# Kernel optimization log

Hardware: AMD Instinct MI355X
Metric: run time of the kernel (lower is better)

## Reference

```python
import jax, jax.numpy as jnp
import numpy as np

D_MODEL = 1024
N_HEADS = 16
D_K = D_MODEL // N_HEADS
THETA = 10000.0
BATCH, SEQ = 4, 2048


def apply_rope(x, pos, theta=THETA):
    # x: [B, H, S, d_k]; pos: [S] int. Rotate interleaved pairs (x_{2i}, x_{2i+1}).
    half = x.shape[-1] // 2
    inv_freq = theta ** (-jnp.arange(half, dtype=x.dtype) * 2.0 / x.shape[-1])  # [half]
    ang = pos.astype(x.dtype)[:, None] * inv_freq[None, :]                      # [S, half]
    cos, sin = jnp.cos(ang), jnp.sin(ang)
    x1, x2 = x[..., 0::2], x[..., 1::2]
    r1 = x1 * cos - x2 * sin
    r2 = x1 * sin + x2 * cos
    return jnp.stack([r1, r2], axis=-1).reshape(x.shape)


def setup_inputs() -> dict:
    key = jax.random.key(0)
    k1, k2, k3 = jax.random.split(key, 3)
    x = jax.random.normal(k1, (BATCH, SEQ, D_MODEL), dtype=jnp.float32)
    W_qkv = jax.random.normal(k2, (3 * D_MODEL, D_MODEL), dtype=jnp.float32) * (D_MODEL ** -0.5)
    b_qkv = jnp.zeros((3 * D_MODEL,), dtype=jnp.float32)
    W_o = jax.random.normal(k3, (D_MODEL, D_MODEL), dtype=jnp.float32) * (D_MODEL ** -0.5)
    b_o = jnp.zeros((D_MODEL,), dtype=jnp.float32)
    token_positions = jnp.arange(SEQ, dtype=jnp.int64 if jax.config.jax_enable_x64 else jnp.int32)
    return {"x": x, "token_positions": token_positions, "W_qkv": W_qkv,
            "b_qkv": b_qkv, "W_o": W_o, "b_o": b_o}


def reference(x, token_positions, W_qkv, b_qkv, W_o, b_o):
    B, S, _ = x.shape
    qkv = x @ W_qkv.T + b_qkv                                   # [B, S, 3*d_model]
    qkv = qkv.reshape(B, S, 3, N_HEADS, D_K)
    qkv = jnp.transpose(qkv, (2, 0, 3, 1, 4))                   # [3, B, H, S, d_k]
    q, k, v = qkv[0], qkv[1], qkv[2]
    q = apply_rope(q, token_positions)
    k = apply_rope(k, token_positions)
    scores = jnp.einsum('bhqd,bhkd->bhqk', q / jnp.sqrt(jnp.asarray(D_K, x.dtype)), k)
    causal = jnp.tril(jnp.ones((S, S), dtype=bool))             # True where attended
    scores = jnp.where(causal, scores, jnp.asarray(-jnp.inf, scores.dtype))
    attn = jax.nn.softmax(scores, axis=-1)
    out = jnp.einsum('bhqk,bhkd->bhqd', attn, v)                # [B, H, S, d_k]
    out = jnp.transpose(out, (0, 2, 1, 3)).reshape(B, S, D_MODEL)
    return out @ W_o.T + b_o
```

## Files before the change

kernel.cpp:

```cpp
#include <hip/hip_runtime.h>
#include <hip/hip_bf16.h>
#include <cstdint>

#define S_LEN 2048
#define NHEAD 16
#define DMODEL 1024

using short8 = __attribute__((ext_vector_type(8))) short;
using f32x4  = __attribute__((ext_vector_type(4))) float;

__device__ __forceinline__ float bf2f(ushort u) {
    return __uint_as_float(((uint32_t)u) << 16);
}
__device__ __forceinline__ ushort f2bf(float f) {
    uint32_t u = __float_as_uint(f);
    u += 0x7FFF + ((u >> 16) & 1);
    return (ushort)(u >> 16);
}
__device__ __forceinline__ uint32_t cvt_pk_bf16(float lo, float hi) {
    uint32_t r;
    asm("v_cvt_pk_bf16_f32 %0, %1, %2" : "=v"(r) : "v"(lo), "v"(hi));
    return r;
}
__device__ __forceinline__ float exp2_(float x) {
    float r; asm("v_exp_f32 %0, %1" : "=v"(r) : "v"(x)); return r;
}
template<int N> __device__ __forceinline__ void vwait() {
    asm volatile("s_waitcnt vmcnt(%0)" :: "n"(N) : "memory");
}

__global__ void k_cast(const float* __restrict__ in, ushort* __restrict__ out, int n4) {
    int i = blockIdx.x * blockDim.x + threadIdx.x;
    if (i < n4) {
        const float4 v = reinterpret_cast<const float4*>(in)[i];
        ushort4 o;
        o.x = f2bf(v.x); o.y = f2bf(v.y); o.z = f2bf(v.z); o.w = f2bf(v.w);
        reinterpret_cast<ushort4*>(out)[i] = o;
    }
}

__device__ __forceinline__ void gl16(const ushort* g, ushort* l) {
    __builtin_amdgcn_global_load_lds(
        (const __attribute__((address_space(1))) void*)g,
        (__attribute__((address_space(3))) void*)l, 16, 0, 0);
}

__global__ __launch_bounds__(512, 2)
void k_gemm256(const ushort* __restrict__ A, const ushort* __restrict__ Bm,
               const float* __restrict__ bias, ushort* __restrict__ C,
               int M, int N, int K, int nbn)
{
    __shared__ ushort As[2][16384];
    __shared__ ushort Bs[2][16384];

    const int bid = blockIdx.x;
    const int cpx = gridDim.x >> 3;
    const int wg = (bid & 7) * cpx + (bid >> 3);
    const int bn = (wg % nbn) * 256, bm = (wg / nbn) * 256;
    const int t = threadIdx.x, w = t >> 6, l = t & 63;
    const int wr = w >> 2, wc = w & 3;
    const int lr = l & 15, lg = l >> 4;

    f32x4 acc[8][4] = {};

    auto stage_pair = [&](int kt, int b, int u0) {
        #pragma unroll
        for (int uu = 0; uu < 2; ++uu) {
            const int u = u0 + uu;
            const int e = (u & 3) * 4096 + t * 8;
            const int r = e >> 6;
            const int c = (e & 63) ^ ((r & 7) << 3);
            if (u < 4) gl16(Bm + (size_t)(bn + r) * K + kt * 64 + c, &Bs[b][e]);
            else       gl16(A  + (size_t)(bm + r) * K + kt * 64 + c, &As[b][e]);
        }
    };

    const int NT = K >> 6;

    stage_pair(0, 0, 0); stage_pair(0, 0, 2);
    stage_pair(0, 0, 4); stage_pair(0, 0, 6);
    if (NT > 1) {
        stage_pair(1, 1, 0); stage_pair(1, 1, 2);
        vwait<4>();
    } else {
        vwait<0>();
    }
    __builtin_amdgcn_s_barrier();

    short8 bfr[4][2];

    for (int tt = 0; tt < NT; ++tt) {
        const int b = tt & 1;
        const ushort* Al = As[b];
        const ushort* Bl = Bs[b];

        #pragma unroll
        for (int p = 0; p < 4; ++p) {
            if (p == 0) {
                #pragma unroll
                for (int n = 0; n < 4; ++n) {
                    const int rB = wc * 64 + n * 16 + lr;
                    #pragma unroll
                    for (int kk = 0; kk < 2; ++kk)
                        bfr[n][kk] = *(const short8*)&Bl[rB * 64 + ((kk * 32 + lg * 8) ^ ((rB & 7) << 3))];
                }
            }
            short8 afr[2][2];
            #pragma unroll
            for (int jj = 0; jj < 2; ++jj) {
                const int rA = wr * 16 + 32 * (2 * p + jj) + lr;
                #pragma unroll
                for (int kk = 0; kk < 2; ++kk)
                    afr[jj][kk] = *(const short8*)&Al[rA * 64 + ((kk * 32 + lg * 8) ^ ((rA & 7) << 3))];
            }
            if      (p == 0) { if (tt + 1 < NT) stage_pair(tt + 1, b ^ 1, 4); }
            else if (p == 1) { if (tt + 1 < NT) stage_pair(tt + 1, b ^ 1, 6); }
            else if (p == 2) { if (tt + 2 < NT) stage_pair(tt + 2, b, 0); }
            else             { if (tt + 2 < NT) stage_pair(tt + 2, b, 2); }

            __builtin_amdgcn_s_barrier();
            __builtin_amdgcn_s_setprio(1);
            #pragma unroll
            for (int jj = 0; jj < 2; ++jj)
                #pragma unroll
                for (int n = 0; n < 4; ++n)
                    #pragma unroll
                    for (int kk = 0; kk < 2; ++kk)
                        acc[2 * p + jj][n] = __builtin_amdgcn_mfma_f32_16x16x32_bf16(
                            afr[jj][kk], bfr[n][kk], acc[2 * p + jj][n], 0, 0, 0);
            __builtin_amdgcn_s_setprio(0);
            if (p == 3) {
                if      (tt + 2 < NT) vwait<4>();
                else if (tt + 1 < NT) vwait<0>();
            }
            __builtin_amdgcn_s_barrier();
        }
    }

    const int col0 = bn + wc * 64 + lr;
    float bv[4];
    #pragma unroll
    for (int n = 0; n < 4; ++n) bv[n] = bias[col0 + n * 16];
    #pragma unroll
    for (int j = 0; j < 8; ++j) {
        const int row0 = bm + wr * 16 + 32 * j + lg * 4;
        #pragma unroll
        for (int r = 0; r < 4; ++r) {
            const size_t ro = (size_t)(row0 + r) * N;
            #pragma unroll
            for (int n = 0; n < 4; ++n)
                C[ro + col0 + n * 16] = f2bf(acc[j][n][r] + bv[n]);
        }
    }
}

__global__ __launch_bounds__(256, 2)
void k_gemm_bt(const ushort* __restrict__ A, const ushort* __restrict__ Bm,
               const float* __restrict__ bias, float* __restrict__ Cout,
               int M, int N, int K)
{
    __shared__ ushort As[128 * 32];
    __shared__ ushort Bs[128 * 32];
    const int t = threadIdx.x;
    const int w = t >> 6, l = t & 63;
    const int lr = l & 15, lg = l >> 4;
    const int bm = blockIdx.y * 128, bn = blockIdx.x * 128;
    const int wr = (w >> 1) * 64, wc = (w & 1) * 64;

    f32x4 acc[4][4] = {};

    const ushort* ag = A + (size_t)(bm + (t >> 2)) * K + (t & 3) * 8;
    const ushort* bg = Bm + (size_t)(bn + (t >> 2)) * K + (t & 3) * 8;
    ushort* asd = &As[t * 8];
    ushort* bsd = &Bs[t * 8];
    const size_t rowskip = (size_t)64 * K;

    for (int k0 = 0; k0 < K; k0 += 32) {
        gl16(ag + k0, asd);
        gl16(ag + rowskip + k0, asd + 2048);
        gl16(bg + k0, bsd);
        gl16(bg + rowskip + k0, bsd + 2048);
        __syncthreads();
        short8 af[4], bf[4];
        #pragma unroll
        for (int m = 0; m < 4; ++m)
            af[m] = *reinterpret_cast<const short8*>(&As[(wr + m * 16 + lr) * 32 + lg * 8]);
        #pragma unroll
        for (int n = 0; n < 4; ++n)
            bf[n] = *reinterpret_cast<const short8*>(&Bs[(wc + n * 16 + lr) * 32 + lg * 8]);
        #pragma unroll
        for (int m = 0; m < 4; ++m)
            #pragma unroll
            for (int n = 0; n < 4; ++n)
                acc[m][n] = __builtin_amdgcn_mfma_f32_16x16x32_bf16(af[m], bf[n], acc[m][n], 0, 0, 0);
        __syncthreads();
    }

    const int col0 = bn + wc + lr;
    float bv[4];
    #pragma unroll
    for (int n = 0; n < 4; ++n) bv[n] = bias[col0 + n * 16];
    #pragma unroll
    for (int m = 0; m < 4; ++m) {
        const int row0 = bm + wr + m * 16 + lg * 4;
        #pragma unroll
        for (int r = 0; r < 4; ++r) {
            const size_t ro = (size_t)(row0 + r) * N;
            #pragma unroll
            for (int n = 0; n < 4; ++n)
                Cout[ro + col0 + n * 16] = acc[m][n][r] + bv[n];
        }
    }
}

__global__ __launch_bounds__(256)
void k_rope_scatter(const ushort* __restrict__ qkv, const int* __restrict__ pos,
                    ushort* __restrict__ Qo, ushort* __restrict__ Ko, ushort* __restrict__ Vt)
{
    __shared__ ushort vlds[64][72];
    const int blk = blockIdx.x;
    const int st = blk & 31, bh = blk >> 5;
    const int b = bh >> 4, h = bh & 15;
    const int t = threadIdx.x;
    const int sl = t >> 2, dc = (t & 3) << 4;
    const int s = st * 64 + sl;
    const size_t base = (size_t)(b * S_LEN + s) * 3072 + h * 64 + dc;
    const float p = (float)pos[s];

    float cs[8], sn[8];
    #pragma unroll
    for (int j = 0; j < 8; ++j) {
        const int fi = (dc >> 1) + j;
        const float invf = __expf(-(float)fi * 0.28782313662425572f);
        __sincosf(p * invf, &sn[j], &cs[j]);
    }

    #pragma unroll
    for (int type = 0; type < 2; ++type) {
        union { uint4 u[2]; ushort us[16]; } in_, out_;
        in_.u[0] = *(const uint4*)(qkv + base + type * 1024);
        in_.u[1] = *(const uint4*)(qkv + base + type * 1024 + 8);
        const float scale = (type == 0) ? 0.125f * 1.44269504088896f : 1.0f;
        #pragma unroll
        for (int j = 0; j < 8; ++j) {
            float x1 = bf2f(in_.us[2 * j]), x2 = bf2f(in_.us[2 * j + 1]);
            out_.us[2 * j]     = f2bf((x1 * cs[j] - x2 * sn[j]) * scale);
            out_.us[2 * j + 1] = f2bf((x1 * sn[j] + x2 * cs[j]) * scale);
        }
        ushort* dst = (type == 0 ? Qo : Ko) + ((size_t)(bh * S_LEN + s)) * 64 + dc;
        *(uint4*)dst = out_.u[0];
        *(uint4*)(dst + 8) = out_.u[1];
    }

    {
        uint4 v0 = *(const uint4*)(qkv + base + 2048);
        uint4 v1 = *(const uint4*)(qkv + base + 2048 + 8);
        *(uint4*)&vlds[sl][dc] = v0;
        *(uint4*)&vlds[sl][dc + 8] = v1;
    }
    __syncthreads();
    {
        const int d = t >> 2, sc0 = (t & 3) << 4;
        union { uint4 u[2]; ushort us[16]; } o;
        #pragma unroll
        for (int j = 0; j < 16; ++j) o.us[j] = vlds[sc0 + j][d];
        ushort* dst = Vt + ((size_t)bh * 64 + d) * S_LEN + st * 64 + sc0;
        *(uint4*)dst = o.u[0];
        *(uint4*)(dst + 8) = o.u[1];
    }
}

__global__ __launch_bounds__(256, 3)
void k_attn(const ushort* __restrict__ Q, const ushort* __restrict__ Kk,
            const ushort* __restrict__ Vt, ushort* __restrict__ O)
{
    __shared__ ushort Ks[2][4096];
    __shared__ ushort Vs[2][4096];
    __shared__ ushort P[4][32][72];

    const int blk = blockIdx.x;
    const int qb = 15 - (blk >> 6);
    const int bh = blk & 63;
    const int b = bh >> 4, h = bh & 15;
    const int t = threadIdx.x, w = t >> 6, l = t & 63;
    const int lr = l & 15, lg = l >> 4;

    const ushort* Kb = Kk + (size_t)bh * S_LEN * 64;
    const ushort* Vb = Vt + (size_t)bh * 64 * S_LEN;
    const ushort* Qb = Q + (size_t)bh * S_LEN * 64;

    const int qbase0 = qb * 128 + w * 16;
    const int qbase1 = qbase0 + 64;

    short8 qf[2][2];
    #pragma unroll
    for (int qg = 0; qg < 2; ++qg)
        #pragma unroll
        for (int dh = 0; dh < 2; ++dh)
            qf[qg][dh] = *(const short8*)(Qb + (size_t)(qbase0 + qg * 64 + lr) * 64 + dh * 32 + lg * 8);

    f32x4 acc[2][4] = {};
    float mx[2] = {-INFINITY, -INFINITY}, ls[2] = {0.f, 0.f};

    const int nt = 2 * qb + 2;

    auto stage = [&](int kb2, int buf) {
        ushort* Kd = Ks[buf]; ushort* Vd = Vs[buf];
        #pragma unroll
        for (int j = 0; j < 2; ++j) {
            const int e = (j * 256 + t) * 8;
            const int row = e >> 6;
            const int col = (e & 63) ^ ((row & 7) << 3);
            gl16(Kb + (size_t)(kb2 + row) * 64 + col, Kd + e);
            gl16(Vb + (size_t)row * S_LEN + kb2 + col, Vd + e);
        }
    };

    stage(0, 0);
    __syncthreads();

    for (int kt = 0; kt < nt; ++kt) {
        const int cur = kt & 1;
        const int kb = kt * 64;
        if (kt + 1 < nt) stage(kb + 64, cur ^ 1);

        const ushort* Kl = Ks[cur];
        short8 kf[4][2];
        #pragma unroll
        for (int i = 0; i < 4; ++i) {
            const int krow = i * 16 + lr, sw = (krow & 7) << 3;
            kf[i][0] = *(const short8*)&Kl[krow * 64 + ((lg * 8) ^ sw)];
            kf[i][1] = *(const short8*)&Kl[krow * 64 + ((32 + lg * 8) ^ sw)];
        }

        auto do_group = [&](int qg, int qbaseg, bool domask) {
            f32x4 st[4] = {};
            __builtin_amdgcn_s_setprio(1);
            #pragma unroll
            for (int i = 0; i < 4; ++i) {
                st[i] = __builtin_amdgcn_mfma_f32_16x16x32_bf16(kf[i][0], qf[qg][0], st[i], 0, 0, 0);
                st[i] = __builtin_amdgcn_mfma_f32_16x16x32_bf16(kf[i][1], qf[qg][1], st[i], 0, 0, 0);
            }
            __builtin_amdgcn_s_setprio(0);
            if (domask) {
                const int qrow = qbaseg + lr;
                #pragma unroll
                for (int i = 0; i < 4; ++i)
                    #pragma unroll
                    for (int r = 0; r < 4; ++r)
                        if (kb + i * 16 + lg * 4 + r > qrow) st[i][r] = -INFINITY;
            }
            float a0 = fmaxf(fmaxf(st[0][0], st[0][1]), fmaxf(st[0][2], st[0][3]));
            float a1 = fmaxf(fmaxf(st[1][0], st[1][1]), fmaxf(st[1][2], st[1][3]));
            float a2 = fmaxf(fmaxf(st[2][0], st[2][1]), fmaxf(st[2][2], st[2][3]));
            float a3 = fmaxf(fmaxf(st[3][0], st[3][1]), fmaxf(st[3][2], st[3][3]));
            float tm = fmaxf(fmaxf(a0, a1), fmaxf(a2, a3));
            tm = fmaxf(tm, __shfl_xor(tm, 16));
            tm = fmaxf(tm, __shfl_xor(tm, 32));
            float mn = mx[qg];
            if (!__all(tm <= mn + 12.0f)) {
                mn = fmaxf(mx[qg], tm);
                const float sc = exp2_(mx[qg] - mn);
                ls[qg] *= sc;
                #pragma unroll
                for (int d = 0; d < 4; ++d)
                    #pragma unroll
                    for (int r = 0; r < 4; ++r) acc[qg][d][r] *= sc;
                mx[qg] = mn;
            }
            float ps = 0.f;
            #pragma unroll
            for (int i = 0; i < 4; ++i) {
                const float e0 = exp2_(st[i][0] - mn);
                const float e1 = exp2_(st[i][1] - mn);
                const float e2 = exp2_(st[i][2] - mn);
                const float e3 = exp2_(st[i][3] - mn);
                ps += (e0 + e1) + (e2 + e3);
                uint2 pk;
                pk.x = cvt_pk_bf16(e0, e1);
                pk.y = cvt_pk_bf16(e2, e3);
                *(uint2*)&P[w][qg * 16 + lr][i * 16 + lg * 4] = pk;
            }
            ps += __shfl_xor(ps, 16);
            ps += __shfl_xor(ps, 32);
            ls[qg] += ps;
        };

        const bool g0 = (kt < nt - 1);
        do_group(1, qbase1, kt == nt - 1);
        if (g0) do_group(0, qbase0, kt == nt - 2);

        short8 pf1[2], pf0[2];
        pf1[0] = *(const short8*)&P[w][16 + lr][lg * 8];
        pf1[1] = *(const short8*)&P[w][16 + lr][32 + lg * 8];
        if (g0) {
            pf0[0] = *(const short8*)&P[w][lr][lg * 8];
            pf0[1] = *(const short8*)&P[w][lr][32 + lg * 8];
        }
        const ushort* Vl = Vs[cur];
        __builtin_amdgcn_s_setprio(1);
        #pragma unroll
        for (int d = 0; d < 4; ++d) {
            const int vrow = d * 16 + lr, sw = (vrow & 7) << 3;
            short8 v0 = *(const short8*)&Vl[vrow * 64 + ((lg * 8) ^ sw)];
            short8 v1 = *(const short8*)&Vl[vrow * 64 + ((32 + lg * 8) ^ sw)];
            acc[1][d] = __builtin_amdgcn_mfma_f32_16x16x32_bf16(v0, pf1[0], acc[1][d], 0, 0, 0);
            acc[1][d] = __builtin_amdgcn_mfma_f32_16x16x32_bf16(v1, pf1[1], acc[1][d], 0, 0, 0);
            if (g0) {
                acc[0][d] = __builtin_amdgcn_mfma_f32_16x16x32_bf16(v0, pf0[0], acc[0][d], 0, 0, 0);
                acc[0][d] = __builtin_amdgcn_mfma_f32_16x16x32_bf16(v1, pf0[1], acc[0][d], 0, 0, 0);
            }
        }
        __builtin_amdgcn_s_setprio(0);
        __syncthreads();
    }

    #pragma unroll
    for (int qg = 0; qg < 2; ++qg) {
        const float inv = 1.f / ls[qg];
        const int q = qbase0 + qg * 64 + lr;
        #pragma unroll
        for (int d = 0; d < 4; ++d) {
            ushort4 ov;
            #pragma unroll
            for (int r = 0; r < 4; ++r) ((ushort*)&ov)[r] = f2bf(acc[qg][d][r] * inv);
            *(ushort4*)&O[((size_t)(b * S_LEN) + q) * 1024 + h * 64 + d * 16 + lg * 4] = ov;
        }
    }
}

extern "C" void kernel_launch(void* const* d_in, const int* in_sizes, int n_in,
                              void* d_out, int out_size, void* d_ws, size_t ws_size,
                              hipStream_t stream)
{
    const float* x    = (const float*)d_in[0];
    const int*   pos  = (const int*)d_in[1];
    const float* Wqkv = (const float*)d_in[2];
    const float* bqkv = (const float*)d_in[3];
    const float* Wo   = (const float*)d_in[4];
    const float* bo   = (const float*)d_in[5];
    float* out = (float*)d_out;

    char* ws = (char*)d_ws;
    ushort* xb   = (ushort*)(ws);
    ushort* wqb  = (ushort*)(ws + 16777216);
    ushort* wob  = (ushort*)(ws + 23068672);
    ushort* qkvb = (ushort*)(ws + 25165824);
    ushort* Qb   = (ushort*)(ws + 75497472);
    ushort* Kb   = (ushort*)(ws + 92274688);
    ushort* Vtb  = (ushort*)(ws + 109051904);
    ushort* AOb  = (ushort*)(ws + 125829120);

    k_cast<<<8192, 256, 0, stream>>>(x, xb, 2097152);
    k_cast<<<3072, 256, 0, stream>>>(Wqkv, wqb, 786432);
    k_cast<<<1024, 256, 0, stream>>>(Wo, wob, 262144);
    k_gemm256<<<384, 512, 0, stream>>>(xb, wqb, bqkv, qkvb, 8192, 3072, 1024, 12);
    k_rope_scatter<<<2048, 256, 0, stream>>>(qkvb, pos, Qb, Kb, Vtb);
    k_attn<<<1024, 256, 0, stream>>>(Qb, Kb, Vtb, AOb);
    k_gemm_bt<<<dim3(8, 64), 256, 0, stream>>>(AOb, wob, bo, out, 8192, 1024, 1024);
}
```

Baseline: 188.8 us.

## Software-pipeline LDS fragment reads with MFMA via double-buffered registers

```diff
diff --git a/kernel.cpp b/kernel.cpp
--- a/kernel.cpp
+++ b/kernel.cpp
@@ -77,64 +77,72 @@
 
     const int NT = K >> 6;
 
+    short8 bC[4][2], bN[4][2], aC[2][2], aN[2][2];
+
+    auto rdB = [&](short8 (&dst)[4][2], const ushort* Bl) {
+        #pragma unroll
+        for (int n = 0; n < 4; ++n) {
+            const int rB = wc * 64 + n * 16 + lr;
+            #pragma unroll
+            for (int kk = 0; kk < 2; ++kk)
+                dst[n][kk] = *(const short8*)&Bl[rB * 64 + ((kk * 32 + lg * 8) ^ ((rB & 7) << 3))];
+        }
+    };
+    auto rdA = [&](short8 (&dst)[2][2], const ushort* Al, int p) {
+        #pragma unroll
+        for (int jj = 0; jj < 2; ++jj) {
+            const int rA = wr * 16 + 32 * (2 * p + jj) + lr;
+            #pragma unroll
+            for (int kk = 0; kk < 2; ++kk)
+                dst[jj][kk] = *(const short8*)&Al[rA * 64 + ((kk * 32 + lg * 8) ^ ((rA & 7) << 3))];
+        }
+    };
+    auto mf = [&](short8 (&a)[2][2], short8 (&bb)[4][2], int p) {
+        __builtin_amdgcn_s_setprio(1);
+        #pragma unroll
+        for (int jj = 0; jj < 2; ++jj)
+            #pragma unroll
+            for (int n = 0; n < 4; ++n)
+                #pragma unroll
+                for (int kk = 0; kk < 2; ++kk)
+                    acc[2 * p + jj][n] = __builtin_amdgcn_mfma_f32_16x16x32_bf16(
+                        a[jj][kk], bb[n][kk], acc[2 * p + jj][n], 0, 0, 0);
+        __builtin_amdgcn_s_setprio(0);
+    };
+
     stage_pair(0, 0, 0); stage_pair(0, 0, 2);
     stage_pair(0, 0, 4); stage_pair(0, 0, 6);
-    if (NT > 1) {
-        stage_pair(1, 1, 0); stage_pair(1, 1, 2);
-        vwait<4>();
-    } else {
-        vwait<0>();
-    }
+    stage_pair(1, 1, 0); stage_pair(1, 1, 2);
+    vwait<4>();
     __builtin_amdgcn_s_barrier();
-
-    short8 bfr[4][2];
-
-    for (int tt = 0; tt < NT; ++tt) {
-        const int b = tt & 1;
-        const ushort* Al = As[b];
-        const ushort* Bl = Bs[b];
-
-        #pragma unroll
-        for (int p = 0; p < 4; ++p) {
-            if (p == 0) {
-                #pragma unroll
-                for (int n = 0; n < 4; ++n) {
-                    const int rB = wc * 64 + n * 16 + lr;
-                    #pragma unroll
-                    for (int kk = 0; kk < 2; ++kk)
-                        bfr[n][kk] = *(const short8*)&Bl[rB * 64 + ((kk * 32 + lg * 8) ^ ((rB & 7) << 3))];
-                }
-            }
-            short8 afr[2][2];
-            #pragma unroll
-            for (int jj = 0; jj < 2; ++jj) {
-                const int rA = wr * 16 + 32 * (2 * p + jj) + lr;
-                #pragma unroll
-                for (int kk = 0; kk < 2; ++kk)
-                    afr[jj][kk] = *(const short8*)&Al[rA * 64 + ((kk * 32 + lg * 8) ^ ((rA & 7) << 3))];
-            }
-            if      (p == 0) { if (tt + 1 < NT) stage_pair(tt + 1, b ^ 1, 4); }
-            else if (p == 1) { if (tt + 1 < NT) stage_pair(tt + 1, b ^ 1, 6); }
-            else if (p == 2) { if (tt + 2 < NT) stage_pair(tt + 2, b, 0); }
-            else             { if (tt + 2 < NT) stage_pair(tt + 2, b, 2); }
-
-            __builtin_amdgcn_s_barrier();
-            __builtin_amdgcn_s_setprio(1);
-            #pragma unroll
-            for (int jj = 0; jj < 2; ++jj)
-                #pragma unroll
-                for (int n = 0; n < 4; ++n)
-                    #pragma unroll
-                    for (int kk = 0; kk < 2; ++kk)
-                        acc[2 * p + jj][n] = __builtin_amdgcn_mfma_f32_16x16x32_bf16(
-                            afr[jj][kk], bfr[n][kk], acc[2 * p + jj][n], 0, 0, 0);
-            __builtin_amdgcn_s_setprio(0);
-            if (p == 3) {
-                if      (tt + 2 < NT) vwait<4>();
-                else if (tt + 1 < NT) vwait<0>();
-            }
-            __builtin_amdgcn_s_barrier();
-        }
+    rdB(bC, Bs[0]);
+    rdA(aC, As[0], 0);
+
+    auto tile = [&](int tt, const ushort* Al, const ushort* Bl,
+                    const ushort* AlN, const ushort* BlN, int b,
+                    short8 (&bCur)[4][2], short8 (&bNxt)[4][2]) {
+        if (tt + 1 < NT) { stage_pair(tt + 1, b ^ 1, 4); stage_pair(tt + 1, b ^ 1, 6); }
+        rdA(aN, Al, 1);
+        mf(aC, bCur, 0);
+        __builtin_amdgcn_s_barrier();
+        if (tt + 2 < NT) stage_pair(tt + 2, b, 0);
+        rdA(aC, Al, 2);
+        mf(aN, bCur, 1);
+        __builtin_amdgcn_s_barrier();
+        if (tt + 2 < NT) stage_pair(tt + 2, b, 2);
+        rdA(aN, Al, 3);
+        mf(aC, bCur, 2);
+        if      (tt + 2 < NT) vwait<4>();
+        else if (tt + 1 < NT) vwait<0>();
+        __builtin_amdgcn_s_barrier();
+        if (tt + 1 < NT) { rdB(bNxt, BlN); rdA(aC, AlN, 0); }
+        mf(aN, bCur, 3);
+        __builtin_amdgcn_s_barrier();
+    };
+
+    for (int tt = 0; tt < NT; tt += 2) {
+        tile(tt,     As[0], Bs[0], As[1], Bs[1], 0, bC, bN);
+        tile(tt + 1, As[1], Bs[1], As[0], Bs[0], 1, bN, bC);
     }
 
     const int col0 = bn + wc * 64 + lr;
```

New measurement: 204.5 us. +8.3%, slower.

## Fuse RoPE and head scatter into QKV GEMM epilogue, keep V transpose separate

Applied to the files above, without the earlier changes.

```diff
diff --git a/kernel.cpp b/kernel.cpp
--- a/kernel.cpp
+++ b/kernel.cpp
@@ -47,8 +47,9 @@
 
 __global__ __launch_bounds__(512, 2)
 void k_gemm256(const ushort* __restrict__ A, const ushort* __restrict__ Bm,
-               const float* __restrict__ bias, ushort* __restrict__ C,
-               int M, int N, int K, int nbn)
+               const float* __restrict__ bias, const int* __restrict__ pos,
+               ushort* __restrict__ Qo, ushort* __restrict__ Ko,
+               ushort* __restrict__ Vr, int K, int nbn)
 {
     __shared__ ushort As[2][16384];
     __shared__ ushort Bs[2][16384];
@@ -141,16 +142,79 @@
     float bv[4];
     #pragma unroll
     for (int n = 0; n < 4; ++n) bv[n] = bias[col0 + n * 16];
-    #pragma unroll
-    for (int j = 0; j < 8; ++j) {
-        const int row0 = bm + wr * 16 + 32 * j + lg * 4;
-        #pragma unroll
-        for (int r = 0; r < 4; ++r) {
-            const size_t ro = (size_t)(row0 + r) * N;
-            #pragma unroll
-            for (int n = 0; n < 4; ++n)
-                C[ro + col0 + n * 16] = f2bf(acc[j][n][r] + bv[n]);
-        }
+
+    const int typ = bn >> 10;
+    if (typ < 2) {
+        ushort* Out = (typ == 0) ? Qo : Ko;
+        const float scl = (typ == 0) ? 0.18033688f : 1.0f;
+        const int h = ((bn & 1023) >> 6) + wc;
+        float invf[4];
+        #pragma unroll
+        for (int n = 0; n < 4; ++n)
+            invf[n] = exp2_(-(float)(n * 8 + (lr >> 1)) * 0.41524101186092f);
+        #pragma unroll
+        for (int j = 0; j < 8; ++j) {
+            const int row0 = bm + wr * 16 + 32 * j + lg * 4;
+            #pragma unroll
+            for (int r = 0; r < 4; ++r) {
+                const int row = row0 + r;
+                const int s = row & 2047;
+                const float p = (float)pos[s];
+                const size_t obase = ((size_t)((row >> 11) * NHEAD + h) * S_LEN + s) * 64;
+                #pragma unroll
+                for (int n = 0; n < 4; ++n) {
+                    const float v = acc[j][n][r] + bv[n];
+                    const float prt = __shfl_xor(v, 1);
+                    float sA, cA;
+                    __sincosf(p * invf[n], &sA, &cA);
+                    const float res = (lr & 1) ? (prt * sA + v * cA)
+                                               : (v * cA - prt * sA);
+                    Out[obase + n * 16 + lr] = f2bf(res * scl);
+                }
+            }
+        }
+    } else {
+        const int vcol0 = (bn & 1023) + wc * 64 + lr;
+        #pragma unroll
+        for (int j = 0; j < 8; ++j) {
+            const int row0 = bm + wr * 16 + 32 * j + lg * 4;
+            #pragma unroll
+            for (int r = 0; r < 4; ++r) {
+                const size_t ro = (size_t)(row0 + r) * 1024;
+                #pragma unroll
+                for (int n = 0; n < 4; ++n)
+                    Vr[ro + vcol0 + n * 16] = f2bf(acc[j][n][r] + bv[n]);
+            }
+        }
+    }
+}
+
+__global__ __launch_bounds__(256)
+void k_vtrans(const ushort* __restrict__ Vr, ushort* __restrict__ Vt)
+{
+    __shared__ ushort vlds[64][72];
+    const int blk = blockIdx.x;
+    const int st = blk & 31, bh = blk >> 5;
+    const int b = bh >> 4, h = bh & 15;
+    const int t = threadIdx.x;
+    const int sl = t >> 2, dc = (t & 3) << 4;
+    const int s = st * 64 + sl;
+    const size_t base = (size_t)(b * S_LEN + s) * 1024 + h * 64 + dc;
+    {
+        uint4 v0 = *(const uint4*)(Vr + base);
+        uint4 v1 = *(const uint4*)(Vr + base + 8);
+        *(uint4*)&vlds[sl][dc] = v0;
+        *(uint4*)&vlds[sl][dc + 8] = v1;
+    }
+    __syncthreads();
+    {
+        const int d = t >> 2, sc0 = (t & 3) << 4;
+        union { uint4 u[2]; ushort us[16]; } o;
+        #pragma unroll
+        for (int j = 0; j < 16; ++j) o.us[j] = vlds[sc0 + j][d];
+        ushort* dst = Vt + ((size_t)bh * 64 + d) * S_LEN + st * 64 + sc0;
+        *(uint4*)dst = o.u[0];
+        *(uint4*)(dst + 8) = o.u[1];
     }
 }
 
@@ -213,63 +277,6 @@
     }
 }
 
-__global__ __launch_bounds__(256)
-void k_rope_scatter(const ushort* __restrict__ qkv, const int* __restrict__ pos,
-                    ushort* __restrict__ Qo, ushort* __restrict__ Ko, ushort* __restrict__ Vt)
-{
-    __shared__ ushort vlds[64][72];
-    const int blk = blockIdx.x;
-    const int st = blk & 31, bh = blk >> 5;
-    const int b = bh >> 4, h = bh & 15;
-    const int t = threadIdx.x;
-    const int sl = t >> 2, dc = (t & 3) << 4;
-    const int s = st * 64 + sl;
-    const size_t base = (size_t)(b * S_LEN + s) * 3072 + h * 64 + dc;
-    const float p = (float)pos[s];
-
-    float cs[8], sn[8];
-    #pragma unroll
-    for (int j = 0; j < 8; ++j) {
-        const int fi = (dc >> 1) + j;
-        const float invf = __expf(-(float)fi * 0.28782313662425572f);
-        __sincosf(p * invf, &sn[j], &cs[j]);
-    }
-
-    #pragma unroll
-    for (int type = 0; type < 2; ++type) {
-        union { uint4 u[2]; ushort us[16]; } in_, out_;
-        in_.u[0] = *(const uint4*)(qkv + base + type * 1024);
-        in_.u[1] = *(const uint4*)(qkv + base + type * 1024 + 8);
-        const float scale = (type == 0) ? 0.125f * 1.44269504088896f : 1.0f;
-        #pragma unroll
-        for (int j = 0; j < 8; ++j) {
-            float x1 = bf2f(in_.us[2 * j]), x2 = bf2f(in_.us[2 * j + 1]);
-            out_.us[2 * j]     = f2bf((x1 * cs[j] - x2 * sn[j]) * scale);
-            out_.us[2 * j + 1] = f2bf((x1 * sn[j] + x2 * cs[j]) * scale);
-        }
-        ushort* dst = (type == 0 ? Qo : Ko) + ((size_t)(bh * S_LEN + s)) * 64 + dc;
-        *(uint4*)dst = out_.u[0];
-        *(uint4*)(dst + 8) = out_.u[1];
-    }
-
-    {
-        uint4 v0 = *(const uint4*)(qkv + base + 2048);
-        uint4 v1 = *(const uint4*)(qkv + base + 2048 + 8);
-        *(uint4*)&vlds[sl][dc] = v0;
-        *(uint4*)&vlds[sl][dc + 8] = v1;
-    }
-    __syncthreads();
-    {
-        const int d = t >> 2, sc0 = (t & 3) << 4;
-        union { uint4 u[2]; ushort us[16]; } o;
-        #pragma unroll
-        for (int j = 0; j < 16; ++j) o.us[j] = vlds[sc0 + j][d];
-        ushort* dst = Vt + ((size_t)bh * 64 + d) * S_LEN + st * 64 + sc0;
-        *(uint4*)dst = o.u[0];
-        *(uint4*)(dst + 8) = o.u[1];
-    }
-}
-
 __global__ __launch_bounds__(256, 3)
 void k_attn(const ushort* __restrict__ Q, const ushort* __restrict__ Kk,
             const ushort* __restrict__ Vt, ushort* __restrict__ O)
@@ -445,7 +452,7 @@
     ushort* xb   = (ushort*)(ws);
     ushort* wqb  = (ushort*)(ws + 16777216);
     ushort* wob  = (ushort*)(ws + 23068672);
-    ushort* qkvb = (ushort*)(ws + 25165824);
+    ushort* Vrb  = (ushort*)(ws + 25165824);
     ushort* Qb   = (ushort*)(ws + 75497472);
     ushort* Kb   = (ushort*)(ws + 92274688);
     ushort* Vtb  = (ushort*)(ws + 109051904);
@@ -454,8 +461,8 @@
     k_cast<<<8192, 256, 0, stream>>>(x, xb, 2097152);
     k_cast<<<3072, 256, 0, stream>>>(Wqkv, wqb, 786432);
     k_cast<<<1024, 256, 0, stream>>>(Wo, wob, 262144);
-    k_gemm256<<<384, 512, 0, stream>>>(xb, wqb, bqkv, qkvb, 8192, 3072, 1024, 12);
-    k_rope_scatter<<<2048, 256, 0, stream>>>(qkvb, pos, Qb, Kb, Vtb);
+    k_gemm256<<<384, 512, 0, stream>>>(xb, wqb, bqkv, pos, Qb, Kb, Vrb, 1024, 12);
+    k_vtrans<<<2048, 256, 0, stream>>>(Vrb, Vtb);
     k_attn<<<1024, 256, 0, stream>>>(Qb, Kb, Vtb, AOb);
     k_gemm_bt<<<dim3(8, 64), 256, 0, stream>>>(AOb, wob, bo, out, 8192, 1024, 1024);
 }
```

After: 185.4 us. No clear change (-1.8%).
